# Kernel optimization log

Measured on AMD Instinct MI355X. Metric: run time of the kernel, lower is better.

Reference implementation:

```python
import jax, jax.numpy as jnp
import numpy as np

N_NODES = 50000
N_EDGES = 800000
IN_DIM = 128
NUM_HEADS = 8
OUT_DIM = 16  # per-head dim; NUM_HEADS*OUT_DIM == IN_DIM


def setup_inputs() -> dict:
    key = jax.random.key(0)
    ks = jax.random.split(key, 9)
    s = 1.0 / np.sqrt(IN_DIM)
    return {
        "h": jax.random.normal(ks[0], (N_NODES, IN_DIM), dtype=jnp.float32),
        "src": jax.random.randint(ks[1], (N_EDGES,), 0, N_NODES),
        "dst": jax.random.randint(ks[2], (N_EDGES,), 0, N_NODES),
        "WQ": jax.random.normal(ks[3], (IN_DIM, NUM_HEADS * OUT_DIM), dtype=jnp.float32) * s,
        "bQ": jnp.zeros((NUM_HEADS * OUT_DIM,), dtype=jnp.float32),
        "WK": jax.random.normal(ks[4], (IN_DIM, NUM_HEADS * OUT_DIM), dtype=jnp.float32) * s,
        "bK": jnp.zeros((NUM_HEADS * OUT_DIM,), dtype=jnp.float32),
        "WV": jax.random.normal(ks[5], (IN_DIM, NUM_HEADS * OUT_DIM), dtype=jnp.float32) * s,
        "bV": jnp.zeros((NUM_HEADS * OUT_DIM,), dtype=jnp.float32),
    }


def reference(h, src, dst, WQ, bQ, WK, bK, WV, bV):
    N = h.shape[0]
    # node projections -> [N, H, D]
    Q = (h @ WQ + bQ).reshape(N, NUM_HEADS, OUT_DIM)
    K = (h @ WK + bK).reshape(N, NUM_HEADS, OUT_DIM)
    V = (h @ WV + bV).reshape(N, NUM_HEADS, OUT_DIM)
    # edge-wise score: (K_src * Q_dst) summed over D, scaled by sqrt(D)
    inv_scale = 1.0 / np.sqrt(OUT_DIM)
    score = jnp.einsum("ehd,ehd->eh", K[src], Q[dst]) * inv_scale  # [E, H]
    score_soft = jnp.exp(jnp.clip(score, -5.0, 5.0))[..., None]    # [E, H, 1]
    # scatter-sum messages to destination nodes
    wV = jax.ops.segment_sum(V[src] * score_soft, dst, num_segments=N)  # [N, H, D]
    z = jax.ops.segment_sum(score_soft, dst, num_segments=N)            # [N, H, 1]
    return wV / (z + 1e-6)
```

## Files before the change

### kernel.cpp

```cpp
#include <hip/hip_runtime.h>
#include <hip/hip_bf16.h>

#define IN_DIM 128
#define NUM_HEADS 8
#define OUT_DIM 16

#define BKT_SHIFT 7
#define BKT_MASK 127
#define NB_MAX 512
#define SLAB_SHIFT 13

typedef unsigned int uint;
typedef unsigned short ushort;
using short8 = __attribute__((ext_vector_type(8))) short;
using f32x4  = __attribute__((ext_vector_type(4))) float;
using u32x2  = __attribute__((ext_vector_type(2))) uint;

__device__ inline uint cvt_pk_bf16(float a, float b) {
    uint r;
    asm("v_cvt_pk_bf16_f32 %0, %1, %2" : "=v"(r) : "v"(a), "v"(b));
    return r;
}

__global__ __launch_bounds__(256) void prep_kernel(const float* __restrict__ WQ,
                                                   const float* __restrict__ WK,
                                                   const float* __restrict__ WV,
                                                   ushort* __restrict__ WT,
                                                   int* __restrict__ bucketCursor) {
    const int t = threadIdx.x;
    if (blockIdx.x == 24) {
        for (int i = t; i < NB_MAX; i += 256) bucketCursor[i] = 0;
        return;
    }
    int tid = blockIdx.x * 256 + t;
    int n = tid >> 4;
    int kg = tid & 15;
    const float* W = (n < 128) ? WQ : (n < 256) ? WK : WV;
    int c = n & 127;
    union { short8 s; uint u[4]; } o;
    #pragma unroll
    for (int j = 0; j < 4; ++j) {
        float v0 = W[(kg * 8 + 2 * j) * 128 + c];
        float v1 = W[(kg * 8 + 2 * j + 1) * 128 + c];
        o.u[j] = cvt_pk_bf16(v0, v1);
    }
    *(short8*)(WT + (size_t)n * 128 + kg * 8) = o.s;
}

__global__ __launch_bounds__(256) void stage_kernel(const int* __restrict__ src,
                                                    const int* __restrict__ dst,
                                                    int* __restrict__ bucketCursor,
                                                    uint* __restrict__ slab,
                                                    int nEdges, int nb) {
    __shared__ int cnt[4][NB_MAX];
    __shared__ int base[4][NB_MAX];
    const int t = threadIdx.x;
    const int wv = t >> 6;
    const int e0 = blockIdx.x * 2048;

    for (int i = t; i < 4 * NB_MAX; i += 256) ((int*)cnt)[i] = 0;
    __syncthreads();

    int myDst[8], mySrc[8];
    #pragma unroll
    for (int i = 0; i < 2; ++i) {
        int e = e0 + (i * 256 + t) * 4;
        if (e + 3 < nEdges) {
            int4 d4 = *(const int4*)(dst + e);
            int4 s4 = *(const int4*)(src + e);
            myDst[4*i+0] = d4.x; myDst[4*i+1] = d4.y; myDst[4*i+2] = d4.z; myDst[4*i+3] = d4.w;
            mySrc[4*i+0] = s4.x; mySrc[4*i+1] = s4.y; mySrc[4*i+2] = s4.z; mySrc[4*i+3] = s4.w;
        } else {
            #pragma unroll
            for (int k = 0; k < 4; ++k) {
                int ee = e + k;
                myDst[4*i+k] = (ee < nEdges) ? dst[ee] : -1;
                mySrc[4*i+k] = (ee < nEdges) ? src[ee] : 0;
            }
        }
    }
    #pragma unroll
    for (int i = 0; i < 8; ++i)
        if (myDst[i] >= 0) atomicAdd(&cnt[wv][myDst[i] >> BKT_SHIFT], 1);
    __syncthreads();

    for (int bb = t; bb < NB_MAX; bb += 256) {
        int c0 = cnt[0][bb], c1 = cnt[1][bb], c2 = cnt[2][bb], c3 = cnt[3][bb];
        int tot = c0 + c1 + c2 + c3;
        int gbase = (bb < nb && tot > 0) ? atomicAdd(&bucketCursor[bb], tot) : 0;
        base[0][bb] = gbase;
        base[1][bb] = gbase + c0;
        base[2][bb] = gbase + c0 + c1;
        base[3][bb] = gbase + c0 + c1 + c2;
    }
    __syncthreads();
    for (int i = t; i < 4 * NB_MAX; i += 256) ((int*)cnt)[i] = 0;
    __syncthreads();

    #pragma unroll
    for (int i = 0; i < 8; ++i) {
        int d = myDst[i];
        if (d >= 0) {
            int b = d >> BKT_SHIFT;
            int pos = base[wv][b] + atomicAdd(&cnt[wv][b], 1);
            if (pos < (1 << SLAB_SHIFT))
                slab[((size_t)b << SLAB_SHIFT) + pos] = (uint)mySrc[i] | ((uint)(d & BKT_MASK) << 17);
        }
    }
}

__global__ __launch_bounds__(64, 2) void sort_proj(const uint* __restrict__ slab,
                                                   const int* __restrict__ bucketCursor,
                                                   int* __restrict__ offsets,
                                                   int* __restrict__ srcSorted,
                                                   const float* __restrict__ h,
                                                   const short* __restrict__ WT,
                                                   const float* __restrict__ bQ,
                                                   const float* __restrict__ bK,
                                                   const float* __restrict__ bV,
                                                   uint* __restrict__ Qout,
                                                   uint* __restrict__ KVout,
                                                   int nNodes, int nEdges, int nb) {
    const int t = threadIdx.x;

    if ((int)blockIdx.x < nb) {
        __shared__ int cnt[128];
        __shared__ int sOutBase;
        const int b = blockIdx.x;
        const int count = bucketCursor[b];
        const uint* rec = slab + ((size_t)b << SLAB_SHIFT);

        int acc = 0;
        for (int i = t; i < b; i += 64) acc += bucketCursor[i];
        #pragma unroll
        for (int off = 32; off; off >>= 1) acc += __shfl_down(acc, off);
        if (t == 0) sOutBase = acc;
        cnt[t] = 0; cnt[t + 64] = 0;
        __syncthreads();

        for (int i = t; i < count; i += 64)
            atomicAdd(&cnt[rec[i] >> 17], 1);
        __syncthreads();

        const int outBase = sOutBase;
        int c0 = cnt[2 * t], c1 = cnt[2 * t + 1];
        int s = c0 + c1;
        int x = s;
        #pragma unroll
        for (int off = 1; off < 64; off <<= 1) { int y = __shfl_up(x, off); if (t >= off) x += y; }
        int prefix = x - s;
        int node0 = b << BKT_SHIFT;
        int g0 = node0 + 2 * t, g1 = node0 + 2 * t + 1;
        if (g0 < nNodes) offsets[g0] = outBase + prefix;
        if (g1 < nNodes) offsets[g1] = outBase + prefix + c0;
        __syncthreads();
        cnt[2 * t] = prefix;
        cnt[2 * t + 1] = prefix + c0;
        __syncthreads();

        for (int i = t; i < count; i += 64) {
            uint r = rec[i];
            int pos = atomicAdd(&cnt[r >> 17], 1);
            srcSorted[outBase + pos] = (int)(r & 0x1ffff);
        }
        if (b == 0 && t == 0) offsets[nNodes] = nEdges;
        return;
    }

    const int gw = blockIdx.x - nb;
    const int lane = t;
    const int lr = lane & 15;
    const int q = lane >> 4;
    const int node0 = (gw >> 1) * 64;
    const int chalf = gw & 1;

    short8 a[4][4];
    #pragma unroll
    for (int g = 0; g < 4; ++g) {
        const int row = node0 + g * 16 + lr;
        const bool ok = row < nNodes;
        #pragma unroll
        for (int ks = 0; ks < 4; ++ks) {
            union { short8 s; uint u[4]; } v;
            if (ok) {
                const float* p = h + (size_t)row * 128 + (ks * 4 + q) * 8;
                float4 f0 = *(const float4*)p;
                float4 f1 = *(const float4*)(p + 4);
                v.u[0] = cvt_pk_bf16(f0.x, f0.y);
                v.u[1] = cvt_pk_bf16(f0.z, f0.w);
                v.u[2] = cvt_pk_bf16(f1.x, f1.y);
                v.u[3] = cvt_pk_bf16(f1.z, f1.w);
            } else {
                v.s = (short8)0;
            }
            a[g][ks] = v.s;
        }
    }

    const short8* WT8 = (const short8*)WT;

    #pragma unroll 1
    for (int cc = 0; cc < 4; ++cc) {
        const int c = chalf * 4 + cc;
        const int nq = c * 16 + lr;
        f32x4 aQ[4] = {{0,0,0,0},{0,0,0,0},{0,0,0,0},{0,0,0,0}};
        f32x4 aK[4] = {{0,0,0,0},{0,0,0,0},{0,0,0,0},{0,0,0,0}};
        f32x4 aV[4] = {{0,0,0,0},{0,0,0,0},{0,0,0,0},{0,0,0,0}};
        #pragma unroll
        for (int ks = 0; ks < 4; ++ks) {
            short8 bq = WT8[(size_t)nq * 16 + ks * 4 + q];
            short8 bk = WT8[(size_t)(nq + 128) * 16 + ks * 4 + q];
            short8 bv = WT8[(size_t)(nq + 256) * 16 + ks * 4 + q];
            #pragma unroll
            for (int g = 0; g < 4; ++g) {
                aQ[g] = __builtin_amdgcn_mfma_f32_16x16x32_bf16(a[g][ks], bq, aQ[g], 0, 0, 0);
                aK[g] = __builtin_amdgcn_mfma_f32_16x16x32_bf16(a[g][ks], bk, aK[g], 0, 0, 0);
                aV[g] = __builtin_amdgcn_mfma_f32_16x16x32_bf16(a[g][ks], bv, aV[g], 0, 0, 0);
            }
        }
        const float biasq = bQ[nq];
        const float biask = bK[nq];
        const float biasv = bV[nq];
        #pragma unroll
        for (int g = 0; g < 4; ++g) {
            #pragma unroll
            for (int r = 0; r < 4; ++r) {
                int node = node0 + g * 16 + q * 4 + r;
                float qval = aQ[g][r] + biasq;
                float qpart = __shfl_xor(qval, 1);
                if (node < nNodes) {
                    if ((lr & 1) == 0)
                        Qout[(size_t)node * 64 + (nq >> 1)] = cvt_pk_bf16(qval, qpart);
                    KVout[(size_t)node * 128 + nq] = cvt_pk_bf16(aK[g][r] + biask, aV[g][r] + biasv);
                }
            }
        }
    }
}

__global__ __launch_bounds__(256) void agg_kernel(const int* __restrict__ offsets,
                                                  const int* __restrict__ srcSorted,
                                                  const uint* __restrict__ Q,
                                                  const uint4* __restrict__ KV,
                                                  float* __restrict__ out,
                                                  int nNodes) {
    int wid = (int)((blockIdx.x * (size_t)blockDim.x + threadIdx.x) >> 6);
    if (wid >= nNodes) return;
    const int lane = threadIdx.x & 63;
    const int li = lane & 31;
    const int hf = lane >> 5;
    const int beg = offsets[wid];
    const int end = offsets[wid + 1];

    u32x2 qp = __builtin_nontemporal_load((const u32x2*)(Q + (size_t)wid * 64) + li);
    f32x4 qv;
    qv.x = __uint_as_float(qp.x << 16);
    qv.y = __uint_as_float(qp.x & 0xffff0000u);
    qv.z = __uint_as_float(qp.y << 16);
    qv.w = __uint_as_float(qp.y & 0xffff0000u);

    f32x4 acc = {0.f, 0.f, 0.f, 0.f};
    float zacc = 0.f;

    auto compute = [&](uint4 u, float mask) {
        float k0 = __uint_as_float(u.x << 16), v0 = __uint_as_float(u.x & 0xffff0000u);
        float k1 = __uint_as_float(u.y << 16), v1 = __uint_as_float(u.y & 0xffff0000u);
        float k2 = __uint_as_float(u.z << 16), v2 = __uint_as_float(u.z & 0xffff0000u);
        float k3 = __uint_as_float(u.w << 16), v3 = __uint_as_float(u.w & 0xffff0000u);
        float p = k0 * qv.x + k1 * qv.y + k2 * qv.z + k3 * qv.w;
        p += __shfl_xor(p, 1);
        p += __shfl_xor(p, 2);
        float e = __expf(fminf(fmaxf(p * 0.25f, -5.0f), 5.0f)) * mask;
        acc.x += v0 * e; acc.y += v1 * e; acc.z += v2 * e; acc.w += v3 * e;
        zacc += e;
    };

    int j = beg;
    for (; j + 8 <= end; j += 8) {
        int sI[4];
        #pragma unroll
        for (int i = 0; i < 4; ++i) sI[i] = __builtin_nontemporal_load(srcSorted + j + 2 * i + hf);
        uint4 u[4];
        #pragma unroll
        for (int i = 0; i < 4; ++i) u[i] = KV[(size_t)sI[i] * 32 + li];
        #pragma unroll
        for (int i = 0; i < 4; ++i) compute(u[i], 1.f);
    }
    for (; j + 2 <= end; j += 2) {
        uint4 u = KV[(size_t)srcSorted[j + hf] * 32 + li];
        compute(u, 1.f);
    }
    if (j < end) {
        uint4 u = KV[(size_t)srcSorted[j] * 32 + li];
        compute(u, hf ? 0.f : 1.f);
    }

    acc.x += __shfl_xor(acc.x, 32);
    acc.y += __shfl_xor(acc.y, 32);
    acc.z += __shfl_xor(acc.z, 32);
    acc.w += __shfl_xor(acc.w, 32);
    zacc  += __shfl_xor(zacc, 32);

    if (hf == 0) {
        float inv = 1.0f / (zacc + 1e-6f);
        f32x4 o = {acc.x * inv, acc.y * inv, acc.z * inv, acc.w * inv};
        __builtin_nontemporal_store(o, (f32x4*)(out + (size_t)wid * 128) + li);
    }
}

extern "C" void kernel_launch(void* const* d_in, const int* in_sizes, int n_in,
                              void* d_out, int out_size, void* d_ws, size_t ws_size,
                              hipStream_t stream) {
    const float* h   = (const float*)d_in[0];
    const int*   src = (const int*)d_in[1];
    const int*   dst = (const int*)d_in[2];
    const float* WQ  = (const float*)d_in[3];
    const float* bQ  = (const float*)d_in[4];
    const float* WK  = (const float*)d_in[5];
    const float* bK  = (const float*)d_in[6];
    const float* WV  = (const float*)d_in[7];
    const float* bV  = (const float*)d_in[8];

    const int nNodes = in_sizes[0] / IN_DIM;
    const int nEdges = in_sizes[1];
    const int nb = (nNodes + (1 << BKT_SHIFT) - 1) >> BKT_SHIFT;

    float* out = (float*)d_out;
    const size_t nf = (size_t)nNodes * 128;

    uint*   Qw          = (uint*)d_ws;
    uint*   KVw         = Qw + (size_t)nNodes * 64;
    ushort* WTw         = (ushort*)(KVw + nf);
    int*    bucketCursor= (int*)(WTw + 384 * 128);
    int*    offsets     = bucketCursor + NB_MAX;
    int*    srcSorted   = offsets + (nNodes + 1);
    uint*   slab        = (uint*)(srcSorted + nEdges);

    prep_kernel<<<25, 256, 0, stream>>>(WQ, WK, WV, WTw, bucketCursor);

    int sb = (nEdges + 2047) / 2048;
    stage_kernel<<<sb, 256, 0, stream>>>(src, dst, bucketCursor, slab, nEdges, nb);

    int projWaves = ((nNodes + 63) / 64) * 2;
    sort_proj<<<nb + projWaves, 64, 0, stream>>>(slab, bucketCursor, offsets, srcSorted,
                                                 h, (const short*)WTw, bQ, bK, bV,
                                                 Qw, KVw, nNodes, nEdges, nb);

    int aggBlocks = (nNodes * 64 + 255) / 256;
    agg_kernel<<<aggBlocks, 256, 0, stream>>>(offsets, srcSorted, Qw, (const uint4*)KVw, out, nNodes);
}
```

Baseline: 118.4 us.

## Replace global atomic bucket cursors with deterministic count/scan/scatter passes

Splits the edge bucketing stage into three kernels: a per-block bucket histogram written to a count matrix, a per-bucket exclusive scan over blocks, and a scatter pass that places edges at precomputed offsets. This removes the global atomicAdd contention on bucket cursors and the separate cursor zeroing, and makes slab placement deterministic. In exchange it adds two extra kernel launches, reads the dst array twice, and moves the count and base matrices through global memory. The old overflow guard on slab position is also dropped.

Result: no change. 118.1 us (-0.2%).

```diff
diff --git a/kernel.cpp b/kernel.cpp
--- a/kernel.cpp
+++ b/kernel.cpp
@@ -8,6 +8,7 @@
 #define BKT_SHIFT 7
 #define BKT_MASK 127
 #define NB_MAX 512
+#define SB_MAX 512
 #define SLAB_SHIFT 13
 
 typedef unsigned int uint;
@@ -25,13 +26,8 @@
 __global__ __launch_bounds__(256) void prep_kernel(const float* __restrict__ WQ,
                                                    const float* __restrict__ WK,
                                                    const float* __restrict__ WV,
-                                                   ushort* __restrict__ WT,
-                                                   int* __restrict__ bucketCursor) {
-    const int t = threadIdx.x;
-    if (blockIdx.x == 24) {
-        for (int i = t; i < NB_MAX; i += 256) bucketCursor[i] = 0;
-        return;
-    }
+                                                   ushort* __restrict__ WT) {
+    const int t = threadIdx.x;
     int tid = blockIdx.x * 256 + t;
     int n = tid >> 4;
     int kg = tid & 15;
@@ -47,20 +43,82 @@
     *(short8*)(WT + (size_t)n * 128 + kg * 8) = o.s;
 }
 
-__global__ __launch_bounds__(256) void stage_kernel(const int* __restrict__ src,
-                                                    const int* __restrict__ dst,
-                                                    int* __restrict__ bucketCursor,
-                                                    uint* __restrict__ slab,
-                                                    int nEdges, int nb) {
-    __shared__ int cnt[4][NB_MAX];
-    __shared__ int base[4][NB_MAX];
-    const int t = threadIdx.x;
+__global__ __launch_bounds__(256) void stage_count(const int* __restrict__ dst,
+                                                   int* __restrict__ cntMat,
+                                                   int nEdges, int nb) {
+    __shared__ int cnt[NB_MAX];
+    const int t = threadIdx.x;
+    const int blk = blockIdx.x;
+    for (int i = t; i < NB_MAX; i += 256) cnt[i] = 0;
+    __syncthreads();
+
+    const int e0 = blk * 2048;
+    #pragma unroll
+    for (int i = 0; i < 2; ++i) {
+        int e = e0 + (i * 256 + t) * 4;
+        if (e + 3 < nEdges) {
+            int4 d4 = *(const int4*)(dst + e);
+            atomicAdd(&cnt[d4.x >> BKT_SHIFT], 1);
+            atomicAdd(&cnt[d4.y >> BKT_SHIFT], 1);
+            atomicAdd(&cnt[d4.z >> BKT_SHIFT], 1);
+            atomicAdd(&cnt[d4.w >> BKT_SHIFT], 1);
+        } else {
+            for (int ee = e; ee < nEdges; ++ee) atomicAdd(&cnt[dst[ee] >> BKT_SHIFT], 1);
+        }
+    }
+    __syncthreads();
+    for (int bb = t; bb < nb; bb += 256)
+        cntMat[(size_t)blk * NB_MAX + bb] = cnt[bb];
+}
+
+__global__ __launch_bounds__(256) void bucket_base(const int* __restrict__ cntMat,
+                                                   int* __restrict__ baseMat,
+                                                   int* __restrict__ bucketTotal,
+                                                   int sb) {
+    __shared__ int wsum[4];
+    const int bkt = blockIdx.x;
+    const int t = threadIdx.x;
+    const int lane = t & 63;
     const int wv = t >> 6;
-    const int e0 = blockIdx.x * 2048;
-
-    for (int i = t; i < 4 * NB_MAX; i += 256) ((int*)cnt)[i] = 0;
-    __syncthreads();
-
+
+    int c0 = (2 * t     < sb) ? cntMat[(size_t)(2 * t)     * NB_MAX + bkt] : 0;
+    int c1 = (2 * t + 1 < sb) ? cntMat[(size_t)(2 * t + 1) * NB_MAX + bkt] : 0;
+    int s = c0 + c1;
+    int x = s;
+    #pragma unroll
+    for (int off = 1; off < 64; off <<= 1) { int y = __shfl_up(x, off); if (lane >= off) x += y; }
+    if (lane == 63) wsum[wv] = x;
+    __syncthreads();
+    if (t == 0) {
+        int a = 0;
+        #pragma unroll
+        for (int w = 0; w < 4; ++w) { int tmp = wsum[w]; wsum[w] = a; a += tmp; }
+    }
+    __syncthreads();
+    int prefix = wsum[wv] + (x - s);
+
+    if (2 * t < sb)     baseMat[(size_t)bkt * SB_MAX + 2 * t]     = prefix;
+    if (2 * t + 1 < sb) baseMat[(size_t)bkt * SB_MAX + 2 * t + 1] = prefix + c0;
+    if (t == 255) bucketTotal[bkt] = prefix + s;
+}
+
+__global__ __launch_bounds__(256) void stage_scatter(const int* __restrict__ src,
+                                                     const int* __restrict__ dst,
+                                                     const int* __restrict__ baseMat,
+                                                     uint* __restrict__ slab,
+                                                     int nEdges, int nb) {
+    __shared__ int base[NB_MAX];
+    __shared__ int cur[NB_MAX];
+    const int t = threadIdx.x;
+    const int blk = blockIdx.x;
+
+    for (int bb = t; bb < nb; bb += 256) {
+        base[bb] = baseMat[(size_t)bb * SB_MAX + blk];
+        cur[bb] = 0;
+    }
+    __syncthreads();
+
+    const int e0 = blk * 2048;
     int myDst[8], mySrc[8];
     #pragma unroll
     for (int i = 0; i < 2; ++i) {
@@ -79,38 +137,20 @@
             }
         }
     }
-    #pragma unroll
-    for (int i = 0; i < 8; ++i)
-        if (myDst[i] >= 0) atomicAdd(&cnt[wv][myDst[i] >> BKT_SHIFT], 1);
-    __syncthreads();
-
-    for (int bb = t; bb < NB_MAX; bb += 256) {
-        int c0 = cnt[0][bb], c1 = cnt[1][bb], c2 = cnt[2][bb], c3 = cnt[3][bb];
-        int tot = c0 + c1 + c2 + c3;
-        int gbase = (bb < nb && tot > 0) ? atomicAdd(&bucketCursor[bb], tot) : 0;
-        base[0][bb] = gbase;
-        base[1][bb] = gbase + c0;
-        base[2][bb] = gbase + c0 + c1;
-        base[3][bb] = gbase + c0 + c1 + c2;
-    }
-    __syncthreads();
-    for (int i = t; i < 4 * NB_MAX; i += 256) ((int*)cnt)[i] = 0;
-    __syncthreads();
 
     #pragma unroll
     for (int i = 0; i < 8; ++i) {
         int d = myDst[i];
         if (d >= 0) {
             int b = d >> BKT_SHIFT;
-            int pos = base[wv][b] + atomicAdd(&cnt[wv][b], 1);
-            if (pos < (1 << SLAB_SHIFT))
-                slab[((size_t)b << SLAB_SHIFT) + pos] = (uint)mySrc[i] | ((uint)(d & BKT_MASK) << 17);
+            int r = atomicAdd(&cur[b], 1);
+            slab[((size_t)b << SLAB_SHIFT) + base[b] + r] = (uint)mySrc[i] | ((uint)(d & BKT_MASK) << 17);
         }
     }
 }
 
 __global__ __launch_bounds__(64, 2) void sort_proj(const uint* __restrict__ slab,
-                                                   const int* __restrict__ bucketCursor,
+                                                   const int* __restrict__ bucketTotal,
                                                    int* __restrict__ offsets,
                                                    int* __restrict__ srcSorted,
                                                    const float* __restrict__ h,
@@ -127,11 +167,11 @@
         __shared__ int cnt[128];
         __shared__ int sOutBase;
         const int b = blockIdx.x;
-        const int count = bucketCursor[b];
+        const int count = bucketTotal[b];
         const uint* rec = slab + ((size_t)b << SLAB_SHIFT);
 
         int acc = 0;
-        for (int i = t; i < b; i += 64) acc += bucketCursor[i];
+        for (int i = t; i < b; i += 64) acc += bucketTotal[i];
         #pragma unroll
         for (int off = 32; off; off >>= 1) acc += __shfl_down(acc, off);
         if (t == 0) sOutBase = acc;
@@ -324,25 +364,29 @@
     const int nNodes = in_sizes[0] / IN_DIM;
     const int nEdges = in_sizes[1];
     const int nb = (nNodes + (1 << BKT_SHIFT) - 1) >> BKT_SHIFT;
+    const int sb = (nEdges + 2047) / 2048;
 
     float* out = (float*)d_out;
     const size_t nf = (size_t)nNodes * 128;
 
-    uint*   Qw          = (uint*)d_ws;
-    uint*   KVw         = Qw + (size_t)nNodes * 64;
-    ushort* WTw         = (ushort*)(KVw + nf);
-    int*    bucketCursor= (int*)(WTw + 384 * 128);
-    int*    offsets     = bucketCursor + NB_MAX;
-    int*    srcSorted   = offsets + (nNodes + 1);
-    uint*   slab        = (uint*)(srcSorted + nEdges);
-
-    prep_kernel<<<25, 256, 0, stream>>>(WQ, WK, WV, WTw, bucketCursor);
-
-    int sb = (nEdges + 2047) / 2048;
-    stage_kernel<<<sb, 256, 0, stream>>>(src, dst, bucketCursor, slab, nEdges, nb);
+    uint*   Qw         = (uint*)d_ws;
+    uint*   KVw        = Qw + (size_t)nNodes * 64;
+    ushort* WTw        = (ushort*)(KVw + nf);
+    int*    bucketTotal= (int*)(WTw + 384 * 128);
+    int*    offsets    = bucketTotal + NB_MAX;
+    int*    srcSorted  = offsets + (nNodes + 1);
+    uint*   slab       = (uint*)(srcSorted + nEdges);
+    int*    cntMat     = (int*)(slab + ((size_t)NB_MAX << SLAB_SHIFT));
+    int*    baseMat    = cntMat + (size_t)SB_MAX * NB_MAX;
+
+    prep_kernel<<<24, 256, 0, stream>>>(WQ, WK, WV, WTw);
+
+    stage_count<<<sb, 256, 0, stream>>>(dst, cntMat, nEdges, nb);
+    bucket_base<<<nb, 256, 0, stream>>>(cntMat, baseMat, bucketTotal, sb);
+    stage_scatter<<<sb, 256, 0, stream>>>(src, dst, baseMat, slab, nEdges, nb);
 
     int projWaves = ((nNodes + 63) / 64) * 2;
-    sort_proj<<<nb + projWaves, 64, 0, stream>>>(slab, bucketCursor, offsets, srcSorted,
+    sort_proj<<<nb + projWaves, 64, 0, stream>>>(slab, bucketTotal, offsets, srcSorted,
                                                  h, (const short*)WTw, bQ, bK, bV,
                                                  Qw, KVw, nNodes, nEdges, nb);
 
```
